# Kernel tuning notes

Measured on AMD Instinct MI355X. Metric: run time of the kernel, lower is better.

## Reference

```python
import jax, jax.numpy as jnp
import numpy as np

K = 5       # local window size (odd)
G = 4       # groups

def _gconv1x1(x, w):
    # grouped 1x1 conv: x (b,c,h,w), w (g, c_out_g, c_in_g) -> (b,g,c_out_g,h,w)
    b, c, h, wd = x.shape
    g, co, ci = w.shape
    xg = x.reshape(b, g, ci, h, wd)
    return jnp.einsum('bgihw,goi->bgohw', xg, w)

def _windows(f, h, w):
    # f: (b,g,n,h+2p,w+2p) -> (b,g,n,h,w,K*K), row-major over (ki,kj)
    # matches torch .unfold(2,K,1).unfold(3,K,1).view(..., -1)
    return jnp.stack([f[..., i:i + h, j:j + w]
                      for i in range(K) for j in range(K)], axis=-1)

def setup_inputs() -> dict:
    key = jax.random.key(0)
    k1, k2, k3, k4 = jax.random.split(key, 4)
    x = jax.random.normal(k1, (2, 128, 96, 96), dtype=jnp.float32)
    wq = jax.random.normal(k2, (G, 32, 32), dtype=jnp.float32) * 0.1
    wk = jax.random.normal(k3, (G, 32, 32), dtype=jnp.float32) * 0.1
    wv = jax.random.normal(k4, (G, 32, 32), dtype=jnp.float32) * 0.1
    return {"x": x, "wq": wq, "wk": wk, "wv": wv}

def reference(x, wq, wk, wv):
    b, c, h, w = x.shape
    p = K // 2
    # query: plain grouped 1x1 conv, broadcast over window dim
    q = _gconv1x1(x, wq)[..., None]                      # (b,g,n,h,w,1)
    # key/value: reflect-pad (1x1 conv commutes with padding, same as torch's
    # Conv2d(..., padding=k//2, padding_mode='reflect'))
    xp = jnp.pad(x, ((0, 0), (0, 0), (p, p), (p, p)), mode='reflect')
    kf = _gconv1x1(xp, wk)                               # (b,g,n,h+2p,w+2p)
    vf = _gconv1x1(xp, wv)
    kwin = _windows(kf, h, w)                            # (b,g,n,h,w,K*K)
    vwin = _windows(vf, h, w)
    attn = jax.nn.softmax(q * kwin, axis=-1)             # per-channel window softmax
    y = (attn * vwin).sum(-1)                            # (b,g,n,h,w)
    return y.reshape(b, -1, h, w)                        # (b, c_out, h, w)
```

## Files before the change

kernel.cpp:

```cpp
#include <hip/hip_runtime.h>
#include <hip/hip_bf16.h>


#define HW 96
#define RG 12
#define NPOS 144
#define KVSTR 145

typedef short short8 __attribute__((ext_vector_type(8)));
typedef float float4v __attribute__((ext_vector_type(4)));

__device__ __forceinline__ int refl(int i) {
    i = (i < 0) ? -i : i;
    i = (i > 95) ? (190 - i) : i;
    return i;
}

__device__ __forceinline__ unsigned short f2bf(float f) {
    __hip_bfloat16 h = __float2bfloat16(f);
    return *reinterpret_cast<unsigned short*>(&h);
}
__device__ __forceinline__ float bfbits2f(unsigned int lo16) {
    return __uint_as_float(lo16 << 16);
}

__global__ __launch_bounds__(256, 5) void fused_attn(
    const float* __restrict__ x, const float* __restrict__ wq,
    const float* __restrict__ wk, const float* __restrict__ wv,
    float* __restrict__ out)
{
    __shared__ unsigned short xs[NPOS * 32];
    __shared__ unsigned int   kvb[32 * KVSTR];
    __shared__ unsigned short qs[32 * 64];

    const int tid = threadIdx.x;
    const int g = blockIdx.y, b = blockIdx.z;
    const int h0 = (blockIdx.x / 12) * 8;
    const int w0 = (blockIdx.x % 12) * 8;
    const float* xg = x + (size_t)(b * 128 + g * 32) * (HW * HW);

    #pragma unroll
    for (int it = 0; it < 9; it++) {
        int idx = it * 256 + tid;
        int cp  = idx / NPOS;
        int pos = idx - cp * NPOS;
        int iy = refl(h0 + pos / RG - 2);
        int ix = refl(w0 + pos % RG - 2);
        const float* p = xg + (2 * cp) * (HW * HW) + iy * HW + ix;
        float a = p[0], c = p[HW * HW];
        unsigned int pk = (unsigned int)f2bf(a) | ((unsigned int)f2bf(c) << 16);
        *(unsigned int*)&xs[pos * 32 + 2 * cp] = pk;
    }

    const int wid  = tid >> 6;
    const int lane = tid & 63;
    const int n0   = wid * 8;
    const int col  = lane & 15;
    const int quad = lane >> 4;
    const int koff = quad * 8;

    const float* wrow = (col < 8) ? (wk + (g * 32 + n0 + col) * 32)
                                  : (wv + (g * 32 + n0 + col - 8) * 32);
    short8 bkv;
    #pragma unroll
    for (int j = 0; j < 8; j++)
        ((unsigned short*)&bkv)[j] = f2bf(wrow[koff + j]);

    short8 bq = {0, 0, 0, 0, 0, 0, 0, 0};
    if (col < 8) {
        const float* qr = wq + (g * 32 + n0 + col) * 32;
        #pragma unroll
        for (int j = 0; j < 8; j++)
            ((unsigned short*)&bq)[j] = f2bf(qr[koff + j]);
    }

    __syncthreads();

    #pragma unroll
    for (int t = 0; t < 9; t++) {
        int p = t * 16 + col;
        short8 a = *(const short8*)&xs[p * 32 + koff];
        float4v d = {0.f, 0.f, 0.f, 0.f};
        d = __builtin_amdgcn_mfma_f32_16x16x32_bf16(a, bkv, d, 0, 0, 0);
        int c = n0 + (col & 7);
        unsigned short* dst0 = (unsigned short*)&kvb[c * KVSTR + t * 16 + quad * 4];
        int half = (col < 8) ? 0 : 1;
        #pragma unroll
        for (int r = 0; r < 4; r++)
            dst0[2 * r + half] = f2bf(d[r]);
    }

    #pragma unroll
    for (int t = 0; t < 4; t++) {
        int mp = t * 16 + col;
        int p  = ((mp >> 3) + 2) * RG + (mp & 7) + 2;
        short8 a = *(const short8*)&xs[p * 32 + koff];
        float4v d = {0.f, 0.f, 0.f, 0.f};
        d = __builtin_amdgcn_mfma_f32_16x16x32_bf16(a, bq, d, 0, 0, 0);
        if (col < 8) {
            unsigned int* dst = (unsigned int*)&qs[(n0 + col) * 64 + t * 16 + quad * 4];
            dst[0] = (unsigned int)f2bf(d[0]) | ((unsigned int)f2bf(d[1]) << 16);
            dst[1] = (unsigned int)f2bf(d[2]) | ((unsigned int)f2bf(d[3]) << 16);
        }
    }

    __syncthreads();

    const int ty = lane >> 3, tx = lane & 7;
    float* outp = out + (size_t)((b * 128 + g * 32 + n0) * HW + (h0 + ty)) * HW + (w0 + tx);
    for (int n = 0; n < 8; n++) {
        int c = n0 + n;
        float q = bfbits2f(qs[c * 64 + lane]) * 1.44269504f;
        float den = 0.f, num = 0.f;
        #pragma unroll
        for (int dy = 0; dy < 5; dy++) {
            const unsigned int* rowp = &kvb[c * KVSTR + (ty + dy) * RG + tx];
            #pragma unroll
            for (int dx = 0; dx < 5; dx++) {
                unsigned int u = rowp[dx];
                float kf = __uint_as_float(u << 16);
                float vf = __uint_as_float(u & 0xffff0000u);
                float e;
                asm("v_exp_f32 %0, %1" : "=v"(e) : "v"(q * kf));
                den += e;
                num = fmaf(e, vf, num);
            }
        }
        outp[n * (HW * HW)] = num * __builtin_amdgcn_rcpf(den);
    }
}

extern "C" void kernel_launch(void* const* d_in, const int* in_sizes, int n_in,
                              void* d_out, int out_size, void* d_ws, size_t ws_size,
                              hipStream_t stream) {
    const float* x  = (const float*)d_in[0];
    const float* wq = (const float*)d_in[1];
    const float* wk = (const float*)d_in[2];
    const float* wv = (const float*)d_in[3];
    float* out = (float*)d_out;

    dim3 grid(144, 4, 2);
    fused_attn<<<grid, 256, 0, stream>>>(x, wq, wk, wv, out);
}
```

Measured before the change: 92.73 us.

## Vectorize halo loads with float4, fix reflect edges in LDS, cheapen bf16 rounding

Result: no change. 93.61 us (+1.0%).

```diff
diff --git a/kernel.cpp b/kernel.cpp
--- a/kernel.cpp
+++ b/kernel.cpp
@@ -1,5 +1,4 @@
 #include <hip/hip_runtime.h>
-#include <hip/hip_bf16.h>
 
 
 #define HW 96
@@ -16,15 +15,11 @@
     return i;
 }
 
-__device__ __forceinline__ unsigned short f2bf(float f) {
-    __hip_bfloat16 h = __float2bfloat16(f);
-    return *reinterpret_cast<unsigned short*>(&h);
-}
-__device__ __forceinline__ float bfbits2f(unsigned int lo16) {
-    return __uint_as_float(lo16 << 16);
+__device__ __forceinline__ unsigned int bfr(float f) {
+    return (__float_as_uint(f) + 0x8000u) >> 16;
 }
 
-__global__ __launch_bounds__(256, 5) void fused_attn(
+__global__ __launch_bounds__(256) void fused_attn(
     const float* __restrict__ x, const float* __restrict__ wq,
     const float* __restrict__ wk, const float* __restrict__ wv,
     float* __restrict__ out)
@@ -39,17 +34,24 @@
     const int w0 = (blockIdx.x % 12) * 8;
     const float* xg = x + (size_t)(b * 128 + g * 32) * (HW * HW);
 
+    const int wA   = min(max(w0 - 4, 0), 80);
+    const int colB = wA - w0 + 2;
     #pragma unroll
-    for (int it = 0; it < 9; it++) {
+    for (int it = 0; it < 6; it++) {
         int idx = it * 256 + tid;
-        int cp  = idx / NPOS;
-        int pos = idx - cp * NPOS;
-        int iy = refl(h0 + pos / RG - 2);
-        int ix = refl(w0 + pos % RG - 2);
-        const float* p = xg + (2 * cp) * (HW * HW) + iy * HW + ix;
-        float a = p[0], c = p[HW * HW];
-        unsigned int pk = (unsigned int)f2bf(a) | ((unsigned int)f2bf(c) << 16);
-        *(unsigned int*)&xs[pos * 32 + 2 * cp] = pk;
+        int seg = idx & 3;
+        int pr  = idx >> 2;
+        int ch  = pr & 31;
+        int row = pr >> 5;
+        int iy  = refl(h0 + row - 2);
+        const float4v f4 = *(const float4v*)(xg + ch * (HW * HW) + iy * HW + wA + seg * 4);
+        int col0 = colB + seg * 4;
+        #pragma unroll
+        for (int e = 0; e < 4; e++) {
+            int col = col0 + e;
+            if (col >= 0 && col < RG)
+                xs[(row * RG + col) * 32 + ch] = (unsigned short)bfr(f4[e]);
+        }
     }
 
     const int wid  = tid >> 6;
@@ -64,16 +66,29 @@
     short8 bkv;
     #pragma unroll
     for (int j = 0; j < 8; j++)
-        ((unsigned short*)&bkv)[j] = f2bf(wrow[koff + j]);
+        ((unsigned short*)&bkv)[j] = (unsigned short)bfr(wrow[koff + j]);
 
     short8 bq = {0, 0, 0, 0, 0, 0, 0, 0};
     if (col < 8) {
         const float* qr = wq + (g * 32 + n0 + col) * 32;
         #pragma unroll
         for (int j = 0; j < 8; j++)
-            ((unsigned short*)&bq)[j] = f2bf(qr[koff + j]);
+            ((unsigned short*)&bq)[j] = (unsigned short)bfr(qr[koff + j]);
     }
 
+    if (w0 == 0 || w0 == 88) {
+        __syncthreads();
+        const int left = (w0 == 0);
+        for (int it = 0; it < 3; it++) {
+            int idx = it * 256 + tid;
+            int ch  = idx & 31;
+            int rr  = idx >> 5;
+            int row = rr >> 1, wc = rr & 1;
+            int dstc = left ? wc : (10 + wc);
+            int srcc = left ? (4 - wc) : (8 - wc);
+            xs[(row * RG + dstc) * 32 + ch] = xs[(row * RG + srcc) * 32 + ch];
+        }
+    }
     __syncthreads();
 
     #pragma unroll
@@ -87,7 +102,7 @@
         int half = (col < 8) ? 0 : 1;
         #pragma unroll
         for (int r = 0; r < 4; r++)
-            dst0[2 * r + half] = f2bf(d[r]);
+            dst0[2 * r + half] = (unsigned short)bfr(d[r]);
     }
 
     #pragma unroll
@@ -99,8 +114,12 @@
         d = __builtin_amdgcn_mfma_f32_16x16x32_bf16(a, bq, d, 0, 0, 0);
         if (col < 8) {
             unsigned int* dst = (unsigned int*)&qs[(n0 + col) * 64 + t * 16 + quad * 4];
-            dst[0] = (unsigned int)f2bf(d[0]) | ((unsigned int)f2bf(d[1]) << 16);
-            dst[1] = (unsigned int)f2bf(d[2]) | ((unsigned int)f2bf(d[3]) << 16);
+            unsigned int u0 = __float_as_uint(d[0]) + 0x8000u;
+            unsigned int u1 = __float_as_uint(d[1]) + 0x8000u;
+            unsigned int u2 = __float_as_uint(d[2]) + 0x8000u;
+            unsigned int u3 = __float_as_uint(d[3]) + 0x8000u;
+            dst[0] = __builtin_amdgcn_perm(u1, u0, 0x07060302);
+            dst[1] = __builtin_amdgcn_perm(u3, u2, 0x07060302);
         }
     }
 
@@ -110,7 +129,7 @@
     float* outp = out + (size_t)((b * 128 + g * 32 + n0) * HW + (h0 + ty)) * HW + (w0 + tx);
     for (int n = 0; n < 8; n++) {
         int c = n0 + n;
-        float q = bfbits2f(qs[c * 64 + lane]) * 1.44269504f;
+        float q = __uint_as_float((unsigned int)qs[c * 64 + lane] << 16) * 1.44269504f;
         float den = 0.f, num = 0.f;
         #pragma unroll
         for (int dy = 0; dy < 5; dy++) {
```
